# Kernel tuning notes

Hardware: AMD Instinct MI355X
Metric: run time of the kernel (lower is better)

The kernel has to match this reference:

```python
import jax, jax.numpy as jnp
import numpy as np

S, B, D, H, F, E = 2048, 2, 768, 12, 3072, 8
DH = D // H
T = S * B
CAP = int(2.0 * T / E)  # capacity factor 2.0


def layer_norm(x, g, b, eps=1e-5):
    m = jnp.mean(x, axis=-1, keepdims=True)
    v = jnp.var(x, axis=-1, keepdims=True)
    return (x - m) * jax.lax.rsqrt(v + eps) * g + b


def setup_inputs() -> dict:
    key = jax.random.key(0)
    ks = jax.random.split(key, 16)
    sc = 0.02
    return {
        "src": jax.random.normal(ks[0], (S, B, D), jnp.float32),
        "in_proj_w": sc * jax.random.normal(ks[1], (3 * D, D), jnp.float32),
        "in_proj_b": sc * jax.random.normal(ks[2], (3 * D,), jnp.float32),
        "out_proj_w": sc * jax.random.normal(ks[3], (D, D), jnp.float32),
        "out_proj_b": sc * jax.random.normal(ks[4], (D,), jnp.float32),
        "norm1_g": 1.0 + sc * jax.random.normal(ks[5], (D,), jnp.float32),
        "norm1_b": sc * jax.random.normal(ks[6], (D,), jnp.float32),
        "router_w": sc * jax.random.normal(ks[7], (E, D), jnp.float32),
        "router_b": sc * jax.random.normal(ks[8], (E,), jnp.float32),
        "w1": sc * jax.random.normal(ks[9], (E, D, F), jnp.float32),
        "b1": sc * jax.random.normal(ks[10], (E, F), jnp.float32),
        "w2": sc * jax.random.normal(ks[11], (E, F, D), jnp.float32),
        "b2": sc * jax.random.normal(ks[12], (E, D), jnp.float32),
        "norm2_g": 1.0 + sc * jax.random.normal(ks[13], (D,), jnp.float32),
        "norm2_b": sc * jax.random.normal(ks[14], (D,), jnp.float32),
    }


def reference(src, in_proj_w, in_proj_b, out_proj_w, out_proj_b,
              norm1_g, norm1_b, router_w, router_b, w1, b1, w2, b2,
              norm2_g, norm2_b):
    # ---- multi-head self-attention (dropout = identity, eval mode) ----
    qkv = src @ in_proj_w.T + in_proj_b                # [S,B,3D]
    q, k, v = jnp.split(qkv, 3, axis=-1)

    def heads(t):  # [S,B,D] -> [B,H,S,DH]
        return t.reshape(S, B, H, DH).transpose(1, 2, 0, 3)

    q, k, v = heads(q), heads(k), heads(v)
    scores = jnp.einsum('bhsd,bhtd->bhst', q, k) / np.float32(np.sqrt(DH))
    attn = jax.nn.softmax(scores, axis=-1)
    ctx = jnp.einsum('bhst,bhtd->bhsd', attn, v)       # [B,H,S,DH]
    ctx = ctx.transpose(2, 0, 1, 3).reshape(S, B, D)
    attn_out = ctx @ out_proj_w.T + out_proj_b

    x = layer_norm(src + attn_out, norm1_g, norm1_b)

    # ---- Switch MoE FFN: top-1 routing, capacity-based dispatch ----
    tok = x.reshape(T, D)
    logits = tok @ router_w.T + router_b               # [T,E]
    probs = jax.nn.softmax(logits, axis=-1)
    eidx = jnp.argmax(probs, axis=-1)                  # [T]
    gate = jnp.take_along_axis(probs, eidx[:, None], axis=-1)[:, 0]
    oh = jax.nn.one_hot(eidx, E, dtype=probs.dtype)    # [T,E]
    # position of each token within its expert's queue
    pos = (jnp.cumsum(oh, axis=0) * oh).sum(-1).astype(jnp.int32) - 1

    # scatter tokens into per-expert buffers (tokens over capacity dropped)
    buf = jnp.zeros((E, CAP, D), tok.dtype).at[eidx, pos].set(tok, mode='drop')
    h = jax.nn.relu(jnp.einsum('ecd,edf->ecf', buf, w1) + b1[:, None, :])
    y = jnp.einsum('ecf,efd->ecd', h, w2) + b2[:, None, :]

    keep = pos < CAP
    out_tok = jnp.where(keep[:, None], y[eidx, jnp.minimum(pos, CAP - 1)], 0.0)
    out_tok = out_tok * gate[:, None]
    moe_out = out_tok.reshape(S, B, D)

    # load-balancing loss: E * sum_e(frac_tokens_e * mean_prob_e)
    f = oh.mean(axis=0)
    P = probs.mean(axis=0)
    lb_loss = E * jnp.sum(f * P)

    out = layer_norm(x + moe_out, norm2_g, norm2_b)
    return (out, lb_loss)
```

## Files before the change

kernel.cpp:

```cpp
#include <hip/hip_runtime.h>
#include <hip/hip_bf16.h>


#define S_   2048
#define B_   2
#define D_   768
#define H_   12
#define DH_  64
#define F_   3072
#define E_   8
#define T_   4096
#define CAP_ 1024

#define AP_  68

typedef __hip_bfloat16 bf16;
using short8  = __attribute__((ext_vector_type(8))) short;
using floatx4 = __attribute__((ext_vector_type(4))) float;

__device__ __forceinline__ float b2f(bf16 x) { return __bfloat162float(x); }
__device__ __forceinline__ bf16  f2b(float x) { return __float2bfloat16(x); }

struct SrcF32 { const float* p; };
struct SrcPair { const bf16* h; const bf16* l; };

__device__ __forceinline__ void ld_split(const SrcF32& s, size_t off,
                                         short8& hi, short8& lo) {
  const float* q = s.p + off;
  float4 a = *(const float4*)q;
  float4 b = *(const float4*)(q + 4);
  float va[8] = {a.x, a.y, a.z, a.w, b.x, b.y, b.z, b.w};
  __attribute__((aligned(16))) bf16 h[8], l[8];
#pragma unroll
  for (int j = 0; j < 8; j++) {
    bf16 hh = f2b(va[j]);
    h[j] = hh;
    l[j] = f2b(va[j] - b2f(hh));
  }
  hi = *(const short8*)h; lo = *(const short8*)l;
}
__device__ __forceinline__ void ld_split(const SrcPair& s, size_t off,
                                         short8& hi, short8& lo) {
  hi = *(const short8*)(s.h + off);
  lo = *(const short8*)(s.l + off);
}

template <typename SA, typename SW>
__device__ __forceinline__ void gemm_split_loop(
    const SA& A, const SW& W, int K,
    bf16* AsH, bf16* AsL, bf16* WsH, bf16* WsL, floatx4 (&acc)[4][4]) {
  const int tid = threadIdx.x;
  const int w = tid >> 6, lane = tid & 63;
  const int srow = lane >> 2;
  const int scol = (lane & 3) * 8;
  const int r0 = w * 32 + srow;
  const int lds0 = (w * 32 + srow) * 32 + scol;
  const int wm = (w >> 1) * 64, wn = (w & 1) * 64;
  const int fr = lane & 15, g = lane >> 4;

  for (int kt = 0; kt < K; kt += 32) {
    short8 ah0, al0, ah1, al1, wh0, wl0, wh1, wl1;
    ld_split(A, (size_t)r0 * K + kt + scol, ah0, al0);
    ld_split(A, (size_t)(r0 + 16) * K + kt + scol, ah1, al1);
    ld_split(W, (size_t)r0 * K + kt + scol, wh0, wl0);
    ld_split(W, (size_t)(r0 + 16) * K + kt + scol, wh1, wl1);
    __syncthreads();
    *(short8*)(AsH + lds0)       = ah0;
    *(short8*)(AsH + lds0 + 512) = ah1;
    *(short8*)(AsL + lds0)       = al0;
    *(short8*)(AsL + lds0 + 512) = al1;
    *(short8*)(WsH + lds0)       = wh0;
    *(short8*)(WsH + lds0 + 512) = wh1;
    *(short8*)(WsL + lds0)       = wl0;
    *(short8*)(WsL + lds0 + 512) = wl1;
    __syncthreads();
    short8 afh[4], afl[4], bfh[4], bfl[4];
#pragma unroll
    for (int mi = 0; mi < 4; mi++) {
      int o = (wm + mi * 16 + fr) * 32 + g * 8;
      afh[mi] = *(const short8*)&AsH[o];
      afl[mi] = *(const short8*)&AsL[o];
    }
#pragma unroll
    for (int ni = 0; ni < 4; ni++) {
      int o = (wn + ni * 16 + fr) * 32 + g * 8;
      bfh[ni] = *(const short8*)&WsH[o];
      bfl[ni] = *(const short8*)&WsL[o];
    }
#pragma unroll
    for (int mi = 0; mi < 4; mi++)
#pragma unroll
      for (int ni = 0; ni < 4; ni++) {
        floatx4 z = acc[mi][ni];
        z = __builtin_amdgcn_mfma_f32_16x16x32_bf16(afh[mi], bfh[ni], z, 0, 0, 0);
        z = __builtin_amdgcn_mfma_f32_16x16x32_bf16(afh[mi], bfl[ni], z, 0, 0, 0);
        z = __builtin_amdgcn_mfma_f32_16x16x32_bf16(afl[mi], bfh[ni], z, 0, 0, 0);
        acc[mi][ni] = z;
      }
  }
}

__global__ __launch_bounds__(256) void gemm_split_pairout(
    SrcF32 A, SrcF32 W, const float* __restrict__ bias,
    bf16* __restrict__ Chi, bf16* __restrict__ Clo, int N, int K) {
  __shared__ __attribute__((aligned(16))) bf16 AsH[4096], AsL[4096];
  __shared__ __attribute__((aligned(16))) bf16 WsH[4096], WsL[4096];
  const int m0 = blockIdx.y * 128, n0 = blockIdx.x * 128;
  floatx4 acc[4][4];
#pragma unroll
  for (int i = 0; i < 4; i++)
#pragma unroll
    for (int j = 0; j < 4; j++) acc[i][j] = (floatx4){0.f, 0.f, 0.f, 0.f};
  SrcF32 Aoff{A.p + (size_t)m0 * K};
  SrcF32 Woff{W.p + (size_t)n0 * K};
  gemm_split_loop(Aoff, Woff, K, AsH, AsL, WsH, WsL, acc);

  const int tid = threadIdx.x, w = tid >> 6, lane = tid & 63;
  const int wm = (w >> 1) * 64, wn = (w & 1) * 64;
  const int fr = lane & 15, rg = (lane >> 4) * 4;
#pragma unroll
  for (int mi = 0; mi < 4; mi++) {
#pragma unroll
    for (int ni = 0; ni < 4; ni++) {
      int n = n0 + wn + ni * 16 + fr;
      float bv = bias[n];
#pragma unroll
      for (int r = 0; r < 4; r++) {
        int m = m0 + wm + mi * 16 + rg + r;
        float v = acc[mi][ni][r] + bv;
        bf16 hh = f2b(v);
        Chi[(size_t)m * N + n] = hh;
        Clo[(size_t)m * N + n] = f2b(v - b2f(hh));
      }
    }
  }
}

__global__ __launch_bounds__(256) void gemm_split_f32out(
    SrcPair A, SrcF32 W, const float* __restrict__ bias,
    const float* __restrict__ resid, float* __restrict__ C, int N, int K) {
  __shared__ __attribute__((aligned(16))) bf16 AsH[4096], AsL[4096];
  __shared__ __attribute__((aligned(16))) bf16 WsH[4096], WsL[4096];
  const int m0 = blockIdx.y * 128, n0 = blockIdx.x * 128;
  floatx4 acc[4][4];
#pragma unroll
  for (int i = 0; i < 4; i++)
#pragma unroll
    for (int j = 0; j < 4; j++) acc[i][j] = (floatx4){0.f, 0.f, 0.f, 0.f};
  SrcPair Aoff{A.h + (size_t)m0 * K, A.l + (size_t)m0 * K};
  SrcF32 Woff{W.p + (size_t)n0 * K};
  gemm_split_loop(Aoff, Woff, K, AsH, AsL, WsH, WsL, acc);

  const int tid = threadIdx.x, w = tid >> 6, lane = tid & 63;
  const int wm = (w >> 1) * 64, wn = (w & 1) * 64;
  const int fr = lane & 15, rg = (lane >> 4) * 4;
#pragma unroll
  for (int mi = 0; mi < 4; mi++) {
#pragma unroll
    for (int ni = 0; ni < 4; ni++) {
      int n = n0 + wn + ni * 16 + fr;
      float bv = bias[n];
#pragma unroll
      for (int r = 0; r < 4; r++) {
        int m = m0 + wm + mi * 16 + rg + r;
        C[(size_t)m * N + n] = acc[mi][ni][r] + bv + resid[(size_t)m * N + n];
      }
    }
  }
}

__device__ __forceinline__ void gemm_tile_loop(
    const bf16* __restrict__ Ablk, const bf16* __restrict__ Wblk, int K,
    bf16* As, bf16* Ws, floatx4 (&acc)[4][4]) {
  const int tid = threadIdx.x;
  const int w = tid >> 6, lane = tid & 63;
  const int srow = lane >> 2;
  const int scol = (lane & 3) * 8;
  const bf16* Ag = Ablk + (size_t)(w * 32 + srow) * K + scol;
  const bf16* Wg = Wblk + (size_t)(w * 32 + srow) * K + scol;
  bf16* AsW = As + (w * 32 + srow) * 32 + scol;
  bf16* WsW = Ws + (w * 32 + srow) * 32 + scol;
  const int wm = (w >> 1) * 64, wn = (w & 1) * 64;
  const int fr = lane & 15, g = lane >> 4;

  for (int kt = 0; kt < K; kt += 32) {
    short8 a0 = *(const short8*)(Ag);
    short8 a1 = *(const short8*)(Ag + 16 * (size_t)K);
    short8 w0 = *(const short8*)(Wg);
    short8 w1v = *(const short8*)(Wg + 16 * (size_t)K);
    Ag += 32; Wg += 32;
    __syncthreads();
    *(short8*)(AsW)           = a0;
    *(short8*)(AsW + 16 * 32) = a1;
    *(short8*)(WsW)           = w0;
    *(short8*)(WsW + 16 * 32) = w1v;
    __syncthreads();
    short8 af[4], bfg[4];
#pragma unroll
    for (int mi = 0; mi < 4; mi++)
      af[mi] = *(const short8*)&As[(wm + mi * 16 + fr) * 32 + g * 8];
#pragma unroll
    for (int ni = 0; ni < 4; ni++)
      bfg[ni] = *(const short8*)&Ws[(wn + ni * 16 + fr) * 32 + g * 8];
#pragma unroll
    for (int mi = 0; mi < 4; mi++)
#pragma unroll
      for (int ni = 0; ni < 4; ni++)
        acc[mi][ni] = __builtin_amdgcn_mfma_f32_16x16x32_bf16(
            af[mi], bfg[ni], acc[mi][ni], 0, 0, 0);
  }
}

__global__ __launch_bounds__(256) void moe1_kernel(
    const bf16* __restrict__ xe, const bf16* __restrict__ w1t,
    const float* __restrict__ b1, bf16* __restrict__ h,
    const int* __restrict__ counts) {
  const int e = blockIdx.y >> 3, lt = blockIdx.y & 7;
  int kept = counts[e]; if (kept > CAP_) kept = CAP_;
  if (lt * 128 >= kept) return;
  __shared__ __attribute__((aligned(16))) bf16 As[4096];
  __shared__ __attribute__((aligned(16))) bf16 Ws[4096];
  const int n0 = blockIdx.x * 128;
  floatx4 acc[4][4];
#pragma unroll
  for (int i = 0; i < 4; i++)
#pragma unroll
    for (int j = 0; j < 4; j++) acc[i][j] = (floatx4){0.f, 0.f, 0.f, 0.f};
  gemm_tile_loop(xe + (size_t)(e * CAP_ + lt * 128) * D_,
                 w1t + (size_t)e * F_ * D_ + (size_t)n0 * D_, D_, As, Ws, acc);

  const int tid = threadIdx.x, w = tid >> 6, lane = tid & 63;
  const int wm = (w >> 1) * 64, wn = (w & 1) * 64;
  const int fr = lane & 15, rg = (lane >> 4) * 4;
#pragma unroll
  for (int mi = 0; mi < 4; mi++) {
#pragma unroll
    for (int ni = 0; ni < 4; ni++) {
      int n = n0 + wn + ni * 16 + fr;
      float bv = b1[e * F_ + n];
#pragma unroll
      for (int r = 0; r < 4; r++) {
        int mrow = lt * 128 + wm + mi * 16 + rg + r;
        h[(size_t)(e * CAP_ + mrow) * F_ + n] =
            f2b(fmaxf(acc[mi][ni][r] + bv, 0.f));
      }
    }
  }
}

__global__ __launch_bounds__(256) void moe2_kernel(
    const bf16* __restrict__ h, const bf16* __restrict__ w2t,
    const float* __restrict__ bias2, const int* __restrict__ stok,
    const float* __restrict__ sgate, const int* __restrict__ counts,
    bf16* __restrict__ moe) {
  const int e = blockIdx.y >> 3, lt = blockIdx.y & 7;
  int kept = counts[e]; if (kept > CAP_) kept = CAP_;
  if (lt * 128 >= kept) return;
  __shared__ __attribute__((aligned(16))) bf16 As[4096];
  __shared__ __attribute__((aligned(16))) bf16 Ws[4096];
  const int n0 = blockIdx.x * 128;
  floatx4 acc[4][4];
#pragma unroll
  for (int i = 0; i < 4; i++)
#pragma unroll
    for (int j = 0; j < 4; j++) acc[i][j] = (floatx4){0.f, 0.f, 0.f, 0.f};
  gemm_tile_loop(h + (size_t)(e * CAP_ + lt * 128) * F_,
                 w2t + (size_t)e * D_ * F_ + (size_t)n0 * F_, F_, As, Ws, acc);

  const int tid = threadIdx.x, w = tid >> 6, lane = tid & 63;
  const int wm = (w >> 1) * 64, wn = (w & 1) * 64;
  const int fr = lane & 15, rg = (lane >> 4) * 4;
#pragma unroll
  for (int mi = 0; mi < 4; mi++) {
#pragma unroll
    for (int r = 0; r < 4; r++) {
      int mrow = lt * 128 + wm + mi * 16 + rg + r;
      int slot = e * CAP_ + mrow;
      int t = stok[slot];
      if (t < 0) continue;
      float gt = sgate[slot];
#pragma unroll
      for (int ni = 0; ni < 4; ni++) {
        int n = n0 + wn + ni * 16 + fr;
        moe[(size_t)t * D_ + n] = f2b((acc[mi][ni][r] + bias2[e * D_ + n]) * gt);
      }
    }
  }
}

__global__ __launch_bounds__(256) void vtrans2_kernel(
    const bf16* __restrict__ qh, const bf16* __restrict__ ql,
    bf16* __restrict__ vth, bf16* __restrict__ vtl) {
  __shared__ bf16 th[64][65], tl[64][65];
  const int tid = threadIdx.x;
  const int bh = blockIdx.y, b = bh / H_, hh = bh % H_;
  const int s0 = blockIdx.x * 64;
#pragma unroll
  for (int i = 0; i < 2; i++) {
    int rr = i * 32 + tid / 8, cc = (tid % 8) * 8;
    size_t off = (size_t)((s0 + rr) * B_ + b) * (3 * D_) + 2 * D_ + hh * DH_ + cc;
    short8 vh = *(const short8*)(qh + off);
    short8 vl = *(const short8*)(ql + off);
    const bf16* ph = (const bf16*)&vh;
    const bf16* pl = (const bf16*)&vl;
#pragma unroll
    for (int j = 0; j < 8; j++) { th[rr][cc + j] = ph[j]; tl[rr][cc + j] = pl[j]; }
  }
  __syncthreads();
#pragma unroll
  for (int i = 0; i < 2; i++) {
    int cc = i * 32 + tid / 8, rr = (tid % 8) * 8;
    __attribute__((aligned(16))) bf16 a[8], c[8];
#pragma unroll
    for (int j = 0; j < 8; j++) { a[j] = th[rr + j][cc]; c[j] = tl[rr + j][cc]; }
    size_t off = ((size_t)bh * DH_ + cc) * S_ + s0 + rr;
    *(short8*)(vth + off) = *(const short8*)a;
    *(short8*)(vtl + off) = *(const short8*)c;
  }
}

__global__ __launch_bounds__(256) void attn_kernel(
    const bf16* __restrict__ qh, const bf16* __restrict__ ql,
    const bf16* __restrict__ vth, const bf16* __restrict__ vtl,
    bf16* __restrict__ ch, bf16* __restrict__ cl) {
  __shared__ __attribute__((aligned(16))) bf16 KsH[64 * AP_], KsL[64 * AP_];
  __shared__ __attribute__((aligned(16))) bf16 VsH[64 * AP_], VsL[64 * AP_];
  __shared__ __attribute__((aligned(16))) bf16 PsH[4][16 * AP_], PsL[4][16 * AP_];
  const int tid = threadIdx.x, w = tid >> 6, lane = tid & 63;
  const int bh = blockIdx.y, b = bh / H_, hh = bh % H_;
  const int q0 = blockIdx.x * 64;
  const int fr = lane & 15, g = lane >> 4;

  const int qs = q0 + w * 16 + fr;
  const size_t qoff = (size_t)(qs * B_ + b) * (3 * D_) + hh * DH_;
  const short8 qf0h = *(const short8*)(qh + qoff + g * 8);
  const short8 qf1h = *(const short8*)(qh + qoff + 32 + g * 8);
  const short8 qf0l = *(const short8*)(ql + qoff + g * 8);
  const short8 qf1l = *(const short8*)(ql + qoff + 32 + g * 8);

  float mi_[4], li_[4], alpha[4];
  floatx4 o[4];
#pragma unroll
  for (int r = 0; r < 4; r++) { mi_[r] = -1e30f; li_[r] = 0.f; }
#pragma unroll
  for (int nt = 0; nt < 4; nt++) o[nt] = (floatx4){0.f, 0.f, 0.f, 0.f};

  const int str = tid >> 2;
  const int st16 = (tid & 3) * 16;

  for (int kb = 0; kb < S_ / 64; kb++) {
    const int s0 = kb * 64;
    __syncthreads();
    {
      const size_t koff = (size_t)((s0 + str) * B_ + b) * (3 * D_) + D_ +
                          hh * DH_ + st16;
      *(short8*)&KsH[str * AP_ + st16]     = *(const short8*)(qh + koff);
      *(short8*)&KsH[str * AP_ + st16 + 8] = *(const short8*)(qh + koff + 8);
      *(short8*)&KsL[str * AP_ + st16]     = *(const short8*)(ql + koff);
      *(short8*)&KsL[str * AP_ + st16 + 8] = *(const short8*)(ql + koff + 8);
    }
    {
      const size_t voff = ((size_t)bh * DH_ + str) * S_ + s0 + st16;
      *(short8*)&VsH[str * AP_ + st16]     = *(const short8*)(vth + voff);
      *(short8*)&VsH[str * AP_ + st16 + 8] = *(const short8*)(vth + voff + 8);
      *(short8*)&VsL[str * AP_ + st16]     = *(const short8*)(vtl + voff);
      *(short8*)&VsL[str * AP_ + st16 + 8] = *(const short8*)(vtl + voff + 8);
    }
    __syncthreads();

    floatx4 sc[4];
#pragma unroll
    for (int nt = 0; nt < 4; nt++) {
      int krow = nt * 16 + fr;
      short8 k0h = *(const short8*)&KsH[krow * AP_ + g * 8];
      short8 k1h = *(const short8*)&KsH[krow * AP_ + 32 + g * 8];
      short8 k0l = *(const short8*)&KsL[krow * AP_ + g * 8];
      short8 k1l = *(const short8*)&KsL[krow * AP_ + 32 + g * 8];
      floatx4 z = (floatx4){0.f, 0.f, 0.f, 0.f};
      z = __builtin_amdgcn_mfma_f32_16x16x32_bf16(qf0h, k0h, z, 0, 0, 0);
      z = __builtin_amdgcn_mfma_f32_16x16x32_bf16(qf1h, k1h, z, 0, 0, 0);
      z = __builtin_amdgcn_mfma_f32_16x16x32_bf16(qf0h, k0l, z, 0, 0, 0);
      z = __builtin_amdgcn_mfma_f32_16x16x32_bf16(qf1h, k1l, z, 0, 0, 0);
      z = __builtin_amdgcn_mfma_f32_16x16x32_bf16(qf0l, k0h, z, 0, 0, 0);
      z = __builtin_amdgcn_mfma_f32_16x16x32_bf16(qf1l, k1h, z, 0, 0, 0);
      sc[nt] = z;
    }
#pragma unroll
    for (int nt = 0; nt < 4; nt++)
#pragma unroll
      for (int r = 0; r < 4; r++) sc[nt][r] *= 0.125f;

#pragma unroll
    for (int r = 0; r < 4; r++) {
      float mx = fmaxf(fmaxf(sc[0][r], sc[1][r]), fmaxf(sc[2][r], sc[3][r]));
#pragma unroll
      for (int d = 1; d < 16; d <<= 1) mx = fmaxf(mx, __shfl_xor(mx, d));
      float mn = fmaxf(mi_[r], mx);
      alpha[r] = __expf(mi_[r] - mn);
      float rs = 0.f;
#pragma unroll
      for (int nt = 0; nt < 4; nt++) {
        float p = __expf(sc[nt][r] - mn);
        sc[nt][r] = p; rs += p;
      }
#pragma unroll
      for (int d = 1; d < 16; d <<= 1) rs += __shfl_xor(rs, d);
      li_[r] = li_[r] * alpha[r] + rs;
      mi_[r] = mn;
    }
#pragma unroll
    for (int nt = 0; nt < 4; nt++)
#pragma unroll
      for (int r = 0; r < 4; r++) o[nt][r] *= alpha[r];

    bf16* PwH = &PsH[w][0];
    bf16* PwL = &PsL[w][0];
#pragma unroll
    for (int nt = 0; nt < 4; nt++)
#pragma unroll
      for (int r = 0; r < 4; r++) {
        float p = sc[nt][r];
        bf16 hh2 = f2b(p);
        PwH[((g << 2) + r) * AP_ + nt * 16 + fr] = hh2;
        PwL[((g << 2) + r) * AP_ + nt * 16 + fr] = f2b(p - b2f(hh2));
      }
    __syncthreads();

    short8 p0h = *(const short8*)&PwH[fr * AP_ + g * 8];
    short8 p1h = *(const short8*)&PwH[fr * AP_ + 32 + g * 8];
    short8 p0l = *(const short8*)&PwL[fr * AP_ + g * 8];
    short8 p1l = *(const short8*)&PwL[fr * AP_ + 32 + g * 8];
#pragma unroll
    for (int nt = 0; nt < 4; nt++) {
      int dh = nt * 16 + fr;
      short8 v0h = *(const short8*)&VsH[dh * AP_ + g * 8];
      short8 v1h = *(const short8*)&VsH[dh * AP_ + 32 + g * 8];
      short8 v0l = *(const short8*)&VsL[dh * AP_ + g * 8];
      short8 v1l = *(const short8*)&VsL[dh * AP_ + 32 + g * 8];
      floatx4 z = o[nt];
      z = __builtin_amdgcn_mfma_f32_16x16x32_bf16(p0h, v0h, z, 0, 0, 0);
      z = __builtin_amdgcn_mfma_f32_16x16x32_bf16(p1h, v1h, z, 0, 0, 0);
      z = __builtin_amdgcn_mfma_f32_16x16x32_bf16(p0h, v0l, z, 0, 0, 0);
      z = __builtin_amdgcn_mfma_f32_16x16x32_bf16(p1h, v1l, z, 0, 0, 0);
      z = __builtin_amdgcn_mfma_f32_16x16x32_bf16(p0l, v0h, z, 0, 0, 0);
      z = __builtin_amdgcn_mfma_f32_16x16x32_bf16(p1l, v1h, z, 0, 0, 0);
      o[nt] = z;
    }
  }

#pragma unroll
  for (int nt = 0; nt < 4; nt++) {
#pragma unroll
    for (int r = 0; r < 4; r++) {
      int qrow = q0 + w * 16 + (g << 2) + r;
      float li = fmaxf(li_[r], 1e-20f);
      float v = o[nt][r] / li;
      size_t off = (size_t)(qrow * B_ + b) * D_ + hh * DH_ + nt * 16 + fr;
      bf16 hh2 = f2b(v);
      ch[off] = hh2;
      cl[off] = f2b(v - b2f(hh2));
    }
  }
}

__global__ __launch_bounds__(256) void transpose_kernel(
    const float* __restrict__ src, bf16* __restrict__ dst, int R, int C) {
  __shared__ bf16 tile[64][65];
  const int tid = threadIdx.x;
  const size_t boff = (size_t)blockIdx.z * R * C;
  const int c0 = blockIdx.x * 64, r0 = blockIdx.y * 64;
#pragma unroll
  for (int i = 0; i < 2; i++) {
    int rr = i * 32 + tid / 8, cc = (tid % 8) * 8;
    const float* sp = &src[boff + (size_t)(r0 + rr) * C + c0 + cc];
    float4 v0 = *(const float4*)sp;
    float4 v1 = *(const float4*)(sp + 4);
    tile[rr][cc + 0] = f2b(v0.x); tile[rr][cc + 1] = f2b(v0.y);
    tile[rr][cc + 2] = f2b(v0.z); tile[rr][cc + 3] = f2b(v0.w);
    tile[rr][cc + 4] = f2b(v1.x); tile[rr][cc + 5] = f2b(v1.y);
    tile[rr][cc + 6] = f2b(v1.z); tile[rr][cc + 7] = f2b(v1.w);
  }
  __syncthreads();
#pragma unroll
  for (int i = 0; i < 2; i++) {
    int cc = i * 32 + tid / 8, rr = (tid % 8) * 8;
    __attribute__((aligned(16))) bf16 tmp[8];
#pragma unroll
    for (int j = 0; j < 8; j++) tmp[j] = tile[rr + j][cc];
    *(short8*)&dst[boff + (size_t)(c0 + cc) * R + r0 + rr] =
        *(const short8*)tmp;
  }
}

__global__ __launch_bounds__(256) void ln_kernel(
    const float* __restrict__ x, const bf16* __restrict__ add,
    const float* __restrict__ gam, const float* __restrict__ bet,
    float* __restrict__ out) {
  const int row = blockIdx.x, tid = threadIdx.x;
  float v[3], s = 0.f, sq = 0.f;
#pragma unroll
  for (int j = 0; j < 3; j++) {
    int c = tid + j * 256;
    float t = x[(size_t)row * D_ + c];
    if (add) t += b2f(add[(size_t)row * D_ + c]);
    v[j] = t; s += t; sq += t * t;
  }
#pragma unroll
  for (int d = 1; d < 64; d <<= 1) { s += __shfl_xor(s, d); sq += __shfl_xor(sq, d); }
  __shared__ float ss[4], ssq[4];
  const int w = tid >> 6, lane = tid & 63;
  if (lane == 0) { ss[w] = s; ssq[w] = sq; }
  __syncthreads();
  s = ss[0] + ss[1] + ss[2] + ss[3];
  sq = ssq[0] + ssq[1] + ssq[2] + ssq[3];
  float mean = s * (1.f / D_);
  float var = fmaxf(sq * (1.f / D_) - mean * mean, 0.f);
  float rstd = rsqrtf(var + 1e-5f);
#pragma unroll
  for (int j = 0; j < 3; j++) {
    int c = tid + j * 256;
    out[(size_t)row * D_ + c] = (v[j] - mean) * rstd * gam[c] + bet[c];
  }
}

__global__ __launch_bounds__(256) void router_kernel(
    const float* __restrict__ x, const float* __restrict__ rw,
    const float* __restrict__ rb, float* __restrict__ probs,
    int* __restrict__ eidx, float* __restrict__ gate) {
  const int tid = threadIdx.x, w = tid >> 6, lane = tid & 63;
  const int t = blockIdx.x * 4 + w;
  float acc[E_];
#pragma unroll
  for (int e = 0; e < E_; e++) acc[e] = 0.f;
  for (int j = 0; j < D_ / 64; j++) {
    int c = lane + j * 64;
    float xv = x[(size_t)t * D_ + c];
#pragma unroll
    for (int e = 0; e < E_; e++) acc[e] += xv * rw[e * D_ + c];
  }
#pragma unroll
  for (int e = 0; e < E_; e++)
#pragma unroll
    for (int d = 1; d < 64; d <<= 1) acc[e] += __shfl_xor(acc[e], d);
  if (lane == 0) {
    float lg[E_], p[E_], mx = -1e30f;
#pragma unroll
    for (int e = 0; e < E_; e++) { lg[e] = acc[e] + rb[e]; mx = fmaxf(mx, lg[e]); }
    float sum = 0.f;
#pragma unroll
    for (int e = 0; e < E_; e++) { p[e] = __expf(lg[e] - mx); sum += p[e]; }
    float inv = 1.f / sum;
    int am = 0; float bm = lg[0];
#pragma unroll
    for (int e = 1; e < E_; e++) if (lg[e] > bm) { bm = lg[e]; am = e; }
#pragma unroll
    for (int e = 0; e < E_; e++) probs[t * E_ + e] = p[e] * inv;
    eidx[t] = am;
    gate[t] = p[am] * inv;
  }
}

__global__ __launch_bounds__(512) void router_pos_kernel(
    const int* __restrict__ eidx, const float* __restrict__ probs,
    const float* __restrict__ gate, int* __restrict__ stok,
    float* __restrict__ sgate, int* __restrict__ counts,
    float* __restrict__ lb_out) {
  const int tid = threadIdx.x, e = tid >> 6, lane = tid & 63;
  int base = 0; float sump = 0.f;
  for (int c = 0; c < T_ / 64; c++) {
    int t = c * 64 + lane;
    int ei = eidx[t];
    sump += probs[t * E_ + e];
    bool m = (ei == e);
    unsigned long long mask = __ballot(m);
    if (m) {
      int p = base + (int)__popcll(mask & ((1ull << lane) - 1ull));
      if (p < CAP_) {
        stok[e * CAP_ + p] = t;
        sgate[e * CAP_ + p] = gate[t];
      }
    }
    base += (int)__popcll(mask);
  }
#pragma unroll
  for (int d = 1; d < 64; d <<= 1) sump += __shfl_xor(sump, d);
  __shared__ float sP[E_];
  __shared__ int sC[E_];
  if (lane == 0) { counts[e] = base; sC[e] = base; sP[e] = sump; }
  __syncthreads();
  if (tid == 0) {
    float lb = 0.f;
    for (int i = 0; i < E_; i++) lb += (float)sC[i] * sP[i];
    lb *= (float)E_ / ((float)T_ * (float)T_);
    lb_out[0] = lb;
  }
}

__global__ __launch_bounds__(256) void gather_kernel(
    const float* __restrict__ x, const int* __restrict__ stok,
    bf16* __restrict__ xe) {
  int idx = blockIdx.x * 256 + threadIdx.x;
  int slot = idx / (D_ / 4), r = idx % (D_ / 4);
  int t = stok[slot];
  bf16 o0, o1, o2, o3;
  if (t >= 0) {
    float4 v = *(const float4*)(x + (size_t)t * D_ + r * 4);
    o0 = f2b(v.x); o1 = f2b(v.y); o2 = f2b(v.z); o3 = f2b(v.w);
  } else {
    o0 = o1 = o2 = o3 = f2b(0.f);
  }
  bf16* dst = xe + (size_t)slot * D_ + r * 4;
  dst[0] = o0; dst[1] = o1; dst[2] = o2; dst[3] = o3;
}

extern "C" void kernel_launch(void* const* d_in, const int* in_sizes, int n_in,
                              void* d_out, int out_size, void* d_ws,
                              size_t ws_size, hipStream_t stream) {
  const float* src   = (const float*)d_in[0];
  const float* in_w  = (const float*)d_in[1];
  const float* in_b  = (const float*)d_in[2];
  const float* out_w = (const float*)d_in[3];
  const float* out_b = (const float*)d_in[4];
  const float* n1g   = (const float*)d_in[5];
  const float* n1b   = (const float*)d_in[6];
  const float* rw    = (const float*)d_in[7];
  const float* rb    = (const float*)d_in[8];
  const float* w1    = (const float*)d_in[9];
  const float* b1    = (const float*)d_in[10];
  const float* w2    = (const float*)d_in[11];
  const float* b2p   = (const float*)d_in[12];
  const float* n2g   = (const float*)d_in[13];
  const float* n2b   = (const float*)d_in[14];
  float* out = (float*)d_out;

  char* ws = (char*)d_ws;
  bf16*  qkv_h  = (bf16*)(ws + 0);
  bf16*  qkv_l  = (bf16*)(ws + 18874368);
  bf16*  w1t    = (bf16*)(ws + 0);
  bf16*  w2t    = (bf16*)(ws + 0);
  bf16*  ctx_h  = (bf16*)(ws + 37748736);
  bf16*  ctx_l  = (bf16*)(ws + 44040192);
  bf16*  xe     = (bf16*)(ws + 37748736);
  bf16*  moe    = (bf16*)(ws + 37748736);
  float* xln    = (float*)(ws + 50331648);
  bf16*  vt_h   = (bf16*)(ws + 62914560);
  bf16*  vt_l   = (bf16*)(ws + 69206016);
  bf16*  hbuf   = (bf16*)(ws + 62914560);
  float* probs  = (float*)(ws + 113246208);
  int*   eidx   = (int*)(ws + 113377280);
  float* gate   = (float*)(ws + 113393664);
  int*   counts = (int*)(ws + 113410048);
  int*   stok   = (int*)(ws + 113410304);
  float* sgate  = (float*)(ws + 113443072);

  (void)in_sizes; (void)n_in; (void)out_size; (void)ws_size;

  hipMemsetAsync(stok, 0xFF, E_ * CAP_ * sizeof(int), stream);

  gemm_split_pairout<<<dim3(3 * D_ / 128, T_ / 128), 256, 0, stream>>>(
      SrcF32{src}, SrcF32{in_w}, in_b, qkv_h, qkv_l, 3 * D_, D_);
  vtrans2_kernel<<<dim3(S_ / 64, B_ * H_), 256, 0, stream>>>(
      qkv_h, qkv_l, vt_h, vt_l);
  attn_kernel<<<dim3(S_ / 64, B_ * H_), 256, 0, stream>>>(
      qkv_h, qkv_l, vt_h, vt_l, ctx_h, ctx_l);
  gemm_split_f32out<<<dim3(D_ / 128, T_ / 128), 256, 0, stream>>>(
      SrcPair{ctx_h, ctx_l}, SrcF32{out_w}, out_b, src, xln, D_, D_);
  ln_kernel<<<T_, 256, 0, stream>>>(xln, nullptr, n1g, n1b, xln);
  router_kernel<<<T_ / 4, 256, 0, stream>>>(xln, rw, rb, probs, eidx, gate);
  router_pos_kernel<<<1, 512, 0, stream>>>(eidx, probs, gate, stok, sgate,
                                           counts, out + (size_t)T_ * D_);
  gather_kernel<<<(E_ * CAP_ * (D_ / 4)) / 256, 256, 0, stream>>>(xln, stok, xe);
  transpose_kernel<<<dim3(F_ / 64, D_ / 64, E_), 256, 0, stream>>>(w1, w1t, D_, F_);
  moe1_kernel<<<dim3(F_ / 128, E_ * (CAP_ / 128)), 256, 0, stream>>>(
      xe, w1t, b1, hbuf, counts);
  hipMemsetAsync(moe, 0, (size_t)T_ * D_ * sizeof(bf16), stream);
  transpose_kernel<<<dim3(D_ / 64, F_ / 64, E_), 256, 0, stream>>>(w2, w2t, F_, D_);
  moe2_kernel<<<dim3(D_ / 128, E_ * (CAP_ / 128)), 256, 0, stream>>>(
      hbuf, w2t, b2p, stok, sgate, counts, moe);
  ln_kernel<<<T_, 256, 0, stream>>>(xln, moe, n2g, n2b, out);
}
```

Baseline: 734.5 us.

## Pre-split fp32 inputs to bf16 pairs and register-prefetch next tiles in GEMM/attention

Adds a split kernel that converts src, in_proj_w and out_proj_w to bf16 hi/lo pairs once, instead of splitting inside every GEMM tile load. The GEMM loops and the attention K/V loop now load the next tile into registers right after the LDS store, so global latency overlaps the MFMA work. In attention, a block-wide barrier after the P writes is replaced by an LDS waitcnt, since each wave reads only its own P rows. The cost is extra launches, extra register pressure and extra workspace traffic for the pre-split buffers.

```diff
diff --git a/kernel.cpp b/kernel.cpp
--- a/kernel.cpp
+++ b/kernel.cpp
@@ -21,33 +21,28 @@
 __device__ __forceinline__ float b2f(bf16 x) { return __bfloat162float(x); }
 __device__ __forceinline__ bf16  f2b(float x) { return __float2bfloat16(x); }
 
-struct SrcF32 { const float* p; };
 struct SrcPair { const bf16* h; const bf16* l; };
 
-__device__ __forceinline__ void ld_split(const SrcF32& s, size_t off,
-                                         short8& hi, short8& lo) {
-  const float* q = s.p + off;
-  float4 a = *(const float4*)q;
-  float4 b = *(const float4*)(q + 4);
-  float va[8] = {a.x, a.y, a.z, a.w, b.x, b.y, b.z, b.w};
-  __attribute__((aligned(16))) bf16 h[8], l[8];
-#pragma unroll
-  for (int j = 0; j < 8; j++) {
-    bf16 hh = f2b(va[j]);
-    h[j] = hh;
-    l[j] = f2b(va[j] - b2f(hh));
-  }
-  hi = *(const short8*)h; lo = *(const short8*)l;
-}
-__device__ __forceinline__ void ld_split(const SrcPair& s, size_t off,
-                                         short8& hi, short8& lo) {
-  hi = *(const short8*)(s.h + off);
-  lo = *(const short8*)(s.l + off);
-}
-
-template <typename SA, typename SW>
+__global__ __launch_bounds__(256) void split_kernel(
+    const float* __restrict__ x, bf16* __restrict__ h, bf16* __restrict__ l,
+    int n4) {
+  int i = blockIdx.x * 256 + threadIdx.x;
+  if (i >= n4) return;
+  float4 v = ((const float4*)x)[i];
+  float va[4] = {v.x, v.y, v.z, v.w};
+  __attribute__((aligned(8))) bf16 hh[4], ll[4];
+#pragma unroll
+  for (int j = 0; j < 4; j++) {
+    bf16 t = f2b(va[j]);
+    hh[j] = t;
+    ll[j] = f2b(va[j] - b2f(t));
+  }
+  *(uint2*)(h + (size_t)i * 4) = *(const uint2*)hh;
+  *(uint2*)(l + (size_t)i * 4) = *(const uint2*)ll;
+}
+
 __device__ __forceinline__ void gemm_split_loop(
-    const SA& A, const SW& W, int K,
+    SrcPair A, SrcPair W, int K,
     bf16* AsH, bf16* AsL, bf16* WsH, bf16* WsL, floatx4 (&acc)[4][4]) {
   const int tid = threadIdx.x;
   const int w = tid >> 6, lane = tid & 63;
@@ -58,12 +53,15 @@
   const int wm = (w >> 1) * 64, wn = (w & 1) * 64;
   const int fr = lane & 15, g = lane >> 4;
 
+  size_t o0 = (size_t)r0 * K + scol;
+  size_t o1 = (size_t)(r0 + 16) * K + scol;
+  short8 ah0 = *(const short8*)(A.h + o0), al0 = *(const short8*)(A.l + o0);
+  short8 ah1 = *(const short8*)(A.h + o1), al1 = *(const short8*)(A.l + o1);
+  short8 wh0 = *(const short8*)(W.h + o0), wl0 = *(const short8*)(W.l + o0);
+  short8 wh1 = *(const short8*)(W.h + o1), wl1 = *(const short8*)(W.l + o1);
+
   for (int kt = 0; kt < K; kt += 32) {
-    short8 ah0, al0, ah1, al1, wh0, wl0, wh1, wl1;
-    ld_split(A, (size_t)r0 * K + kt + scol, ah0, al0);
-    ld_split(A, (size_t)(r0 + 16) * K + kt + scol, ah1, al1);
-    ld_split(W, (size_t)r0 * K + kt + scol, wh0, wl0);
-    ld_split(W, (size_t)(r0 + 16) * K + kt + scol, wh1, wl1);
+    o0 += 32; o1 += 32;
     __syncthreads();
     *(short8*)(AsH + lds0)       = ah0;
     *(short8*)(AsH + lds0 + 512) = ah1;
@@ -74,6 +72,12 @@
     *(short8*)(WsL + lds0)       = wl0;
     *(short8*)(WsL + lds0 + 512) = wl1;
     __syncthreads();
+    if (kt + 32 < K) {
+      ah0 = *(const short8*)(A.h + o0); al0 = *(const short8*)(A.l + o0);
+      ah1 = *(const short8*)(A.h + o1); al1 = *(const short8*)(A.l + o1);
+      wh0 = *(const short8*)(W.h + o0); wl0 = *(const short8*)(W.l + o0);
+      wh1 = *(const short8*)(W.h + o1); wl1 = *(const short8*)(W.l + o1);
+    }
     short8 afh[4], afl[4], bfh[4], bfl[4];
 #pragma unroll
     for (int mi = 0; mi < 4; mi++) {
@@ -101,7 +105,7 @@
 }
 
 __global__ __launch_bounds__(256) void gemm_split_pairout(
-    SrcF32 A, SrcF32 W, const float* __restrict__ bias,
+    SrcPair A, SrcPair W, const float* __restrict__ bias,
     bf16* __restrict__ Chi, bf16* __restrict__ Clo, int N, int K) {
   __shared__ __attribute__((aligned(16))) bf16 AsH[4096], AsL[4096];
   __shared__ __attribute__((aligned(16))) bf16 WsH[4096], WsL[4096];
@@ -111,8 +115,8 @@
   for (int i = 0; i < 4; i++)
 #pragma unroll
     for (int j = 0; j < 4; j++) acc[i][j] = (floatx4){0.f, 0.f, 0.f, 0.f};
-  SrcF32 Aoff{A.p + (size_t)m0 * K};
-  SrcF32 Woff{W.p + (size_t)n0 * K};
+  SrcPair Aoff{A.h + (size_t)m0 * K, A.l + (size_t)m0 * K};
+  SrcPair Woff{W.h + (size_t)n0 * K, W.l + (size_t)n0 * K};
   gemm_split_loop(Aoff, Woff, K, AsH, AsL, WsH, WsL, acc);
 
   const int tid = threadIdx.x, w = tid >> 6, lane = tid & 63;
@@ -137,7 +141,7 @@
 }
 
 __global__ __launch_bounds__(256) void gemm_split_f32out(
-    SrcPair A, SrcF32 W, const float* __restrict__ bias,
+    SrcPair A, SrcPair W, const float* __restrict__ bias,
     const float* __restrict__ resid, float* __restrict__ C, int N, int K) {
   __shared__ __attribute__((aligned(16))) bf16 AsH[4096], AsL[4096];
   __shared__ __attribute__((aligned(16))) bf16 WsH[4096], WsL[4096];
@@ -148,7 +152,7 @@
 #pragma unroll
     for (int j = 0; j < 4; j++) acc[i][j] = (floatx4){0.f, 0.f, 0.f, 0.f};
   SrcPair Aoff{A.h + (size_t)m0 * K, A.l + (size_t)m0 * K};
-  SrcF32 Woff{W.p + (size_t)n0 * K};
+  SrcPair Woff{W.h + (size_t)n0 * K, W.l + (size_t)n0 * K};
   gemm_split_loop(Aoff, Woff, K, AsH, AsL, WsH, WsL, acc);
 
   const int tid = threadIdx.x, w = tid >> 6, lane = tid & 63;
@@ -183,11 +187,12 @@
   const int wm = (w >> 1) * 64, wn = (w & 1) * 64;
   const int fr = lane & 15, g = lane >> 4;
 
+  short8 a0 = *(const short8*)(Ag);
+  short8 a1 = *(const short8*)(Ag + 16 * (size_t)K);
+  short8 w0 = *(const short8*)(Wg);
+  short8 w1v = *(const short8*)(Wg + 16 * (size_t)K);
+
   for (int kt = 0; kt < K; kt += 32) {
-    short8 a0 = *(const short8*)(Ag);
-    short8 a1 = *(const short8*)(Ag + 16 * (size_t)K);
-    short8 w0 = *(const short8*)(Wg);
-    short8 w1v = *(const short8*)(Wg + 16 * (size_t)K);
     Ag += 32; Wg += 32;
     __syncthreads();
     *(short8*)(AsW)           = a0;
@@ -195,6 +200,12 @@
     *(short8*)(WsW)           = w0;
     *(short8*)(WsW + 16 * 32) = w1v;
     __syncthreads();
+    if (kt + 32 < K) {
+      a0 = *(const short8*)(Ag);
+      a1 = *(const short8*)(Ag + 16 * (size_t)K);
+      w0 = *(const short8*)(Wg);
+      w1v = *(const short8*)(Wg + 16 * (size_t)K);
+    }
     short8 af[4], bfg[4];
 #pragma unroll
     for (int mi = 0; mi < 4; mi++)
@@ -348,25 +359,43 @@
   const int str = tid >> 2;
   const int st16 = (tid & 3) * 16;
 
+  size_t koff = (size_t)(str * B_ + b) * (3 * D_) + D_ + hh * DH_ + st16;
+  size_t voff = ((size_t)bh * DH_ + str) * S_ + st16;
+  short8 pk0h = *(const short8*)(qh + koff);
+  short8 pk1h = *(const short8*)(qh + koff + 8);
+  short8 pk0l = *(const short8*)(ql + koff);
+  short8 pk1l = *(const short8*)(ql + koff + 8);
+  short8 pv0h = *(const short8*)(vth + voff);
+  short8 pv1h = *(const short8*)(vth + voff + 8);
+  short8 pv0l = *(const short8*)(vtl + voff);
+  short8 pv1l = *(const short8*)(vtl + voff + 8);
+
   for (int kb = 0; kb < S_ / 64; kb++) {
-    const int s0 = kb * 64;
     __syncthreads();
-    {
-      const size_t koff = (size_t)((s0 + str) * B_ + b) * (3 * D_) + D_ +
-                          hh * DH_ + st16;
-      *(short8*)&KsH[str * AP_ + st16]     = *(const short8*)(qh + koff);
-      *(short8*)&KsH[str * AP_ + st16 + 8] = *(const short8*)(qh + koff + 8);
-      *(short8*)&KsL[str * AP_ + st16]     = *(const short8*)(ql + koff);
-      *(short8*)&KsL[str * AP_ + st16 + 8] = *(const short8*)(ql + koff + 8);
-    }
-    {
-      const size_t voff = ((size_t)bh * DH_ + str) * S_ + s0 + st16;
-      *(short8*)&VsH[str * AP_ + st16]     = *(const short8*)(vth + voff);
-      *(short8*)&VsH[str * AP_ + st16 + 8] = *(const short8*)(vth + voff + 8);
-      *(short8*)&VsL[str * AP_ + st16]     = *(const short8*)(vtl + voff);
-      *(short8*)&VsL[str * AP_ + st16 + 8] = *(const short8*)(vtl + voff + 8);
-    }
+    *(short8*)&KsH[str * AP_ + st16]     = pk0h;
+    *(short8*)&KsH[str * AP_ + st16 + 8] = pk1h;
+    *(short8*)&KsL[str * AP_ + st16]     = pk0l;
+    *(short8*)&KsL[str * AP_ + st16 + 8] = pk1l;
+    *(short8*)&VsH[str * AP_ + st16]     = pv0h;
+    *(short8*)&VsH[str * AP_ + st16 + 8] = pv1h;
+    *(short8*)&VsL[str * AP_ + st16]     = pv0l;
+    *(short8*)&VsL[str * AP_ + st16 + 8] = pv1l;
     __syncthreads();
+
+    if (kb + 1 < S_ / 64) {
+      size_t k2 = koff + (size_t)64 * B_ * (3 * D_) * (kb + 1 - kb);
+      koff += (size_t)64 * B_ * (3 * D_);
+      voff += 64;
+      (void)k2;
+      pk0h = *(const short8*)(qh + koff);
+      pk1h = *(const short8*)(qh + koff + 8);
+      pk0l = *(const short8*)(ql + koff);
+      pk1l = *(const short8*)(ql + koff + 8);
+      pv0h = *(const short8*)(vth + voff);
+      pv1h = *(const short8*)(vth + voff + 8);
+      pv0l = *(const short8*)(vtl + voff);
+      pv1l = *(const short8*)(vtl + voff + 8);
+    }
 
     floatx4 sc[4];
 #pragma unroll
@@ -424,7 +453,7 @@
         PwH[((g << 2) + r) * AP_ + nt * 16 + fr] = hh2;
         PwL[((g << 2) + r) * AP_ + nt * 16 + fr] = f2b(p - b2f(hh2));
       }
-    __syncthreads();
+    asm volatile("s_waitcnt lgkmcnt(0)" ::: "memory");
 
     short8 p0h = *(const short8*)&PwH[fr * AP_ + g * 8];
     short8 p1h = *(const short8*)&PwH[fr * AP_ + 32 + g * 8];
@@ -646,6 +675,12 @@
   bf16*  vt_h   = (bf16*)(ws + 62914560);
   bf16*  vt_l   = (bf16*)(ws + 69206016);
   bf16*  hbuf   = (bf16*)(ws + 62914560);
+  bf16*  src_h  = (bf16*)(ws + 75497472);
+  bf16*  src_l  = (bf16*)(ws + 81788928);
+  bf16*  inw_h  = (bf16*)(ws + 88080384);
+  bf16*  inw_l  = (bf16*)(ws + 91619328);
+  bf16*  outw_h = (bf16*)(ws + 95158272);
+  bf16*  outw_l = (bf16*)(ws + 96337920);
   float* probs  = (float*)(ws + 113246208);
   int*   eidx   = (int*)(ws + 113377280);
   float* gate   = (float*)(ws + 113393664);
@@ -657,14 +692,22 @@
 
   hipMemsetAsync(stok, 0xFF, E_ * CAP_ * sizeof(int), stream);
 
+  split_kernel<<<(T_ * D_ / 4) / 256, 256, 0, stream>>>(src, src_h, src_l,
+                                                        T_ * D_ / 4);
+  split_kernel<<<(3 * D_ * D_ / 4) / 256, 256, 0, stream>>>(
+      in_w, inw_h, inw_l, 3 * D_ * D_ / 4);
+  split_kernel<<<(D_ * D_ / 4) / 256, 256, 0, stream>>>(out_w, outw_h, outw_l,
+                                                        D_ * D_ / 4);
+
   gemm_split_pairout<<<dim3(3 * D_ / 128, T_ / 128), 256, 0, stream>>>(
-      SrcF32{src}, SrcF32{in_w}, in_b, qkv_h, qkv_l, 3 * D_, D_);
+      SrcPair{src_h, src_l}, SrcPair{inw_h, inw_l}, in_b, qkv_h, qkv_l,
+      3 * D_, D_);
   vtrans2_kernel<<<dim3(S_ / 64, B_ * H_), 256, 0, stream>>>(
       qkv_h, qkv_l, vt_h, vt_l);
   attn_kernel<<<dim3(S_ / 64, B_ * H_), 256, 0, stream>>>(
       qkv_h, qkv_l, vt_h, vt_l, ctx_h, ctx_l);
   gemm_split_f32out<<<dim3(D_ / 128, T_ / 128), 256, 0, stream>>>(
-      SrcPair{ctx_h, ctx_l}, SrcF32{out_w}, out_b, src, xln, D_, D_);
+      SrcPair{ctx_h, ctx_l}, SrcPair{outw_h, outw_l}, out_b, src, xln, D_, D_);
   ln_kernel<<<T_, 256, 0, stream>>>(xln, nullptr, n1g, n1b, xln);
   router_kernel<<<T_ / 4, 256, 0, stream>>>(xln, rw, rb, probs, eidx, gate);
   router_pos_kernel<<<1, 512, 0, stream>>>(eidx, probs, gate, stok, sgate,
```

New measurement: 703.5 us. 4.2% less time.
